# Performance work log

Hardware: AMD Instinct MI355X
Metric: run time of the kernel (lower is better)

The kernel has to match this reference:

```python
import jax, jax.numpy as jnp
import numpy as np
import math

B, L, M, D, EL, H = 128, 105, 55, 256, 3, 1
PATCH = [3, 5, 7]

def pos_embed(T, d):
    pos = jnp.arange(T, dtype=jnp.float32)[:, None]
    div = jnp.exp(jnp.arange(0, d, 2, dtype=jnp.float32) * (-math.log(10000.0) / d))
    pe = jnp.zeros((T, d), dtype=jnp.float32)
    pe = pe.at[:, 0::2].set(jnp.sin(pos * div))
    pe = pe.at[:, 1::2].set(jnp.cos(pos * div))
    return pe

def circular_conv(x, w):
    # x: [N, T, Cin], w: [Dout, Cin, 3]; Conv1d kernel 3, circular padding 1, no bias
    xc = jnp.pad(x.transpose(0, 2, 1), ((0, 0), (0, 0), (1, 1)), mode='wrap')
    y = jax.lax.conv_general_dilated(xc, w, (1,), 'VALID', dimension_numbers=('NCH', 'OIH', 'NCH'))
    return y.transpose(0, 2, 1)

def _forward(x, conv_p0, conv_n0, conv_p1, conv_n1, conv_p2, conv_n2, Wq, bq, Wk, bk):
    convs = [(conv_p0, conv_n0), (conv_p1, conv_n1), (conv_p2, conv_n2)]
    # RevIN 'norm': per-sample standardization over time; stats are detached in torch
    mean = jax.lax.stop_gradient(jnp.mean(x, axis=1, keepdims=True))
    std = jax.lax.stop_gradient(jnp.sqrt(jnp.var(x, axis=1, keepdims=True) + 1e-5))
    xr = (x - mean) / std                      # [B, L, M]
    xt = xr.transpose(0, 2, 1)                 # [B, M, L]
    dk = D // H
    scale = 1.0 / math.sqrt(dk)
    series_list, prior_list = [], []
    for i, p in enumerate(PATCH):
        n = L // p
        # patch-size branch: (b m) n p -> embed over n with in_channels=p
        x_size = circular_conv(xt.reshape(B * M, n, p), convs[i][0]) + pos_embed(n, D)
        # patch-num branch: (b m) p n -> embed over p with in_channels=n
        x_num = circular_conv(xt.reshape(B * M, p, n), convs[i][1]) + pos_embed(p, D)
        for l in range(EL):
            def attn_mean(z):
                T = z.shape[1]
                q = (z @ Wq[l] + bq[l]).reshape(B * M, T, H, dk)
                k = (z @ Wk[l] + bk[l]).reshape(B * M, T, H, dk)
                a = jax.nn.softmax(scale * jnp.einsum('blhe,bshe->bhls', q, k), axis=-1)
                # fuse: mean over channel BEFORE expanding to window size
                # (repeat/tile commutes with the channel-mean, avoids [B*M,H,L,L])
                return a.reshape(B, M, H, T, T).mean(axis=1)   # [B, H, T, T]
            a_size = attn_mean(x_size)                          # [B, H, n, n]
            # einops repeat '(m rm) (n rn)': element-wise contiguous repeat
            series_list.append(jnp.repeat(jnp.repeat(a_size, p, axis=-2), p, axis=-1))
            a_num = attn_mean(x_num)                            # [B, H, p, p]
            # torch .repeat: tiling
            prior_list.append(jnp.tile(a_num, (1, 1, n, n)))
    # order: patch-major, layer-minor (matches the flattened lists)
    return jnp.stack(series_list), jnp.stack(prior_list)        # each [9, B, H, L, L]

def setup_inputs():
    key = jax.random.key(0)
    ks = jax.random.split(key, 12)
    s = 0.05
    inp = {"x": jax.random.normal(ks[0], (B, L, M), jnp.float32)}
    for i, p in enumerate(PATCH):
        inp[f"conv_p{i}"] = s * jax.random.normal(ks[1 + 2 * i], (D, p, 3), jnp.float32)
        inp[f"conv_n{i}"] = s * jax.random.normal(ks[2 + 2 * i], (D, L // p, 3), jnp.float32)
    inp["Wq"] = s * jax.random.normal(ks[7], (EL, D, D), jnp.float32)
    inp["bq"] = jnp.zeros((EL, D), jnp.float32)
    inp["Wk"] = s * jax.random.normal(ks[8], (EL, D, D), jnp.float32)
    inp["bk"] = jnp.zeros((EL, D), jnp.float32)
    return inp

def reference(x, conv_p0, conv_n0, conv_p1, conv_n1, conv_p2, conv_n2, Wq, bq, Wk, bk):
    return _forward(x, conv_p0, conv_n0, conv_p1, conv_n1, conv_p2, conv_n2, Wq, bq, Wk, bk)
```

## Files before the change

### kernel.cpp

```cpp
#include <hip/hip_runtime.h>
#include <hip/hip_bf16.h>

#define B_ 128
#define L_ 105
#define M_ 55
#define D_ 256
#define NCOMBO 18

#define WS_XT    0
#define WS_PE    739200
#define WS_LEFT  761216
#define WS_RIGHT 1258880
#define WS_MM    1756544
#define WS_MP    761216
#define WS_ACC   1258880
#define LR_STRIDE 27648
#define MM_STRIDE 11664
#define MP_STRIDE 12544
#define ACC_TOT  758016

#define WS_LRP        1966592
#define LRP_KZ_STRIDE 27648
#define LRP_C_STRIDE  110592
#define LRP_HALF      1990656
#define WS_NEED_BYTES ((size_t)(WS_LRP + 2 * LRP_HALF) * 4)

__constant__ int c_peOff[6] = {0, 35, 38, 59, 64, 79};
__constant__ int c_accbase[18] = {0,1225,2450, 3675,3684,3693, 3702,4143,4584,
                                  5025,5050,5075, 5100,5325,5550, 5775,5824,5873};

__device__ __forceinline__ void combo_dims(int c, int& i, int& br, int& l,
                                           int& p, int& n, int& Cin, int& T, int& J) {
    i = c / 6; br = (c % 6) / 3; l = c % 3;
    p = 3 + 2 * i;
    n = L_ / p;
    Cin = br ? n : p;
    T   = br ? p : n;
    J = 3 * Cin;
}

__device__ __forceinline__ float dot4(float4 a, float4 b) {
    return a.x * b.x + a.y * b.y + a.z * b.z + a.w * b.w;
}

__global__ void revin_kernel(const float* __restrict__ x, float* __restrict__ ws) {
    int bm = blockIdx.x; int b = bm / M_; int m = bm % M_;
    int tid = threadIdx.x;
    __shared__ float s1[128], s2[128];
    float v = 0.f;
    if (tid < L_) v = x[(b * L_ + tid) * M_ + m];
    s1[tid] = v; s2[tid] = v * v;
    __syncthreads();
    for (int off = 64; off > 0; off >>= 1) {
        if (tid < off) { s1[tid] += s1[tid + off]; s2[tid] += s2[tid + off]; }
        __syncthreads();
    }
    float mean = s1[0] * (1.f / L_);
    float var  = s2[0] * (1.f / L_) - mean * mean;
    float rstd = rsqrtf(var + 1e-5f);
    if (tid < L_) ws[WS_XT + bm * L_ + tid] = (v - mean) * rstd;
}

__global__ void pe_kernel(float* __restrict__ ws) {
    int bi = blockIdx.x;
    int i = bi / 2, br = bi % 2;
    int p = 3 + 2 * i, n = L_ / p;
    int T = br ? p : n;
    int d = threadIdx.x;
    float divv = expf(-(float)(d & ~1) * (logf(10000.f) / (float)D_));
    float* base = ws + WS_PE + c_peOff[bi] * D_;
    for (int t = 0; t < T; ++t) {
        float arg = (float)t * divv;
        base[t * D_ + d] = (d & 1) ? cosf(arg) : sinf(arg);
    }
}

__global__ __launch_bounds__(256) void lr2_kernel(
                          const float* __restrict__ w0, const float* __restrict__ w1,
                          const float* __restrict__ w2c, const float* __restrict__ w3,
                          const float* __restrict__ w4, const float* __restrict__ w5,
                          const float* __restrict__ Wq, const float* __restrict__ bq,
                          const float* __restrict__ Wk, const float* __restrict__ bk,
                          float* __restrict__ ws) {
    int c = blockIdx.x;
    int i, br, l, p, n, Cin, T, J; combo_dims(c, i, br, l, p, n, Cin, T, J);
    int Mdim = J + T;
    int r0 = blockIdx.y * 8;
    if (r0 >= Mdim) return;
    int kz = blockIdx.z;
    int d0 = kz * 64;
    int wi = i * 2 + br;
    const float* conv = (wi == 0) ? w0 : (wi == 1) ? w1 : (wi == 2) ? w2c
                       : (wi == 3) ? w3 : (wi == 4) ? w4 : w5;
    __shared__ float S[8][64];
    int tid = threadIdx.x;
    for (int idx = tid; idx < 8 * 64; idx += 256) {
        int rr = idx >> 6, dd = idx & 63;
        int row = r0 + rr; float val = 0.f;
        int d = d0 + dd;
        if (row < J) val = conv[d * J + row];
        else if (row < Mdim) val = ws[WS_PE + (c_peOff[wi] + (row - J)) * D_ + d];
        S[rr][dd] = val;
    }
    __syncthreads();
    const float* wqp = Wq + l * D_ * D_;
    const float* wkp = Wk + l * D_ * D_;
    float accL[8], accR[8];
#pragma unroll
    for (int rr = 0; rr < 8; ++rr) { accL[rr] = 0.f; accR[rr] = 0.f; }
    int o = tid;
#pragma unroll 8
    for (int dd = 0; dd < 64; ++dd) {
        int d = d0 + dd;
        float wqv = wqp[d * D_ + o];
        float wkv = wkp[d * D_ + o];
#pragma unroll
        for (int rr = 0; rr < 8; ++rr) {
            float sv = S[rr][dd];
            accL[rr] += sv * wqv;
            accR[rr] += sv * wkv;
        }
    }
    float bqv = (kz == 0) ? bq[l * D_ + o] : 0.f;
    float bkv = (kz == 0) ? bk[l * D_ + o] : 0.f;
    float* Lp = ws + WS_LRP + c * LRP_C_STRIDE + kz * LRP_KZ_STRIDE;
    float* Rp = Lp + LRP_HALF;
#pragma unroll
    for (int rr = 0; rr < 8; ++rr) {
        int row = r0 + rr;
        if (row < Mdim) {
            float aq = (row >= J) ? bqv : 0.f;
            float ak = (row >= J) ? bkv : 0.f;
            Lp[row * D_ + o] = accL[rr] + aq;
            Rp[row * D_ + o] = accR[rr] + ak;
        }
    }
}

__global__ __launch_bounds__(256) void lr_kernel(
                          const float* __restrict__ w0, const float* __restrict__ w1,
                          const float* __restrict__ w2c, const float* __restrict__ w3,
                          const float* __restrict__ w4, const float* __restrict__ w5,
                          const float* __restrict__ Wq, const float* __restrict__ bq,
                          const float* __restrict__ Wk, const float* __restrict__ bk,
                          float* __restrict__ ws) {
    int c = blockIdx.x;
    int i, br, l, p, n, Cin, T, J; combo_dims(c, i, br, l, p, n, Cin, T, J);
    int Mdim = J + T;
    int r0 = blockIdx.y * 4;
    if (r0 >= Mdim) return;
    int wi = i * 2 + br;
    const float* conv = (wi == 0) ? w0 : (wi == 1) ? w1 : (wi == 2) ? w2c
                       : (wi == 3) ? w3 : (wi == 4) ? w4 : w5;
    __shared__ float S[4][256];
    int tid = threadIdx.x;
    for (int idx = tid; idx < 4 * 256; idx += 256) {
        int rr = idx >> 8, dd = idx & 255;
        int row = r0 + rr; float val = 0.f;
        if (row < J) val = conv[dd * J + row];
        else if (row < Mdim) val = ws[WS_PE + (c_peOff[wi] + (row - J)) * D_ + dd];
        S[rr][dd] = val;
    }
    __syncthreads();
    const float* wqp = Wq + l * D_ * D_;
    const float* wkp = Wk + l * D_ * D_;
    float accL[4], accR[4];
#pragma unroll
    for (int rr = 0; rr < 4; ++rr) { accL[rr] = 0.f; accR[rr] = 0.f; }
    int o = tid;
#pragma unroll 8
    for (int d = 0; d < D_; ++d) {
        float wqv = wqp[d * D_ + o];
        float wkv = wkp[d * D_ + o];
#pragma unroll
        for (int rr = 0; rr < 4; ++rr) {
            float sv = S[rr][d];
            accL[rr] += sv * wqv;
            accR[rr] += sv * wkv;
        }
    }
    float bqv = bq[l * D_ + o], bkv = bk[l * D_ + o];
#pragma unroll
    for (int rr = 0; rr < 4; ++rr) {
        int row = r0 + rr;
        if (row < Mdim) {
            float aq = (row >= J) ? bqv : 0.f;
            float ak = (row >= J) ? bkv : 0.f;
            ws[WS_LEFT  + c * LR_STRIDE + row * D_ + o] = accL[rr] + aq;
            ws[WS_RIGHT + c * LR_STRIDE + row * D_ + o] = accR[rr] + ak;
        }
    }
}

__global__ void mm_kernel(float* __restrict__ ws, int use_partial) {
    int c = blockIdx.x;
    int i, br, l, p, n, Cin, T, J; combo_dims(c, i, br, l, p, n, Cin, T, J);
    int Mdim = J + T;
    int tr = blockIdx.y / 7, tc = blockIdx.y % 7;
    int r0 = tr * 16, c0 = tc * 16;
    if (r0 >= Mdim || c0 >= Mdim) return;
    __shared__ __align__(16) float Lb[16][260], Rb[16][260];
    int tid = threadIdx.x;
    if (use_partial) {
        const float* Lp = ws + WS_LRP + c * LRP_C_STRIDE;
        const float* Rp = Lp + LRP_HALF;
        for (int idx = tid; idx < 16 * 256; idx += 256) {
            int rr = idx >> 8, d = idx & 255;
            int rL = r0 + rr, rR = c0 + rr;
            float lv = 0.f, rv = 0.f;
            if (rL < Mdim) {
                int base = rL * D_ + d;
                lv = Lp[base] + Lp[base + LRP_KZ_STRIDE]
                   + Lp[base + 2 * LRP_KZ_STRIDE] + Lp[base + 3 * LRP_KZ_STRIDE];
            }
            if (rR < Mdim) {
                int base = rR * D_ + d;
                rv = Rp[base] + Rp[base + LRP_KZ_STRIDE]
                   + Rp[base + 2 * LRP_KZ_STRIDE] + Rp[base + 3 * LRP_KZ_STRIDE];
            }
            Lb[rr][d] = lv; Rb[rr][d] = rv;
        }
    } else {
        for (int idx = tid; idx < 16 * 256; idx += 256) {
            int rr = idx >> 8, d = idx & 255;
            int rL = r0 + rr, rR = c0 + rr;
            Lb[rr][d] = (rL < Mdim) ? ws[WS_LEFT  + c * LR_STRIDE + rL * D_ + d] : 0.f;
            Rb[rr][d] = (rR < Mdim) ? ws[WS_RIGHT + c * LR_STRIDE + rR * D_ + d] : 0.f;
        }
    }
    __syncthreads();
    int rr = tid / 16, cc = tid % 16;
    const float4* lrow = (const float4*)(&Lb[rr][0]);
    const float4* rrow = (const float4*)(&Rb[cc][0]);
    float acc = 0.f;
#pragma unroll 8
    for (int d4 = 0; d4 < 64; ++d4) {
        float4 a = lrow[d4], bb = rrow[d4];
        acc += a.x * bb.x + a.y * bb.y + a.z * bb.z + a.w * bb.w;
    }
    int r = r0 + rr, cth = c0 + cc;
    if (r < Mdim && cth < Mdim)
        ws[WS_MM + c * MM_STRIDE + r * Mdim + cth] = acc;
}

__global__ void pack_kernel(float* __restrict__ ws) {
    int c = blockIdx.x;
    int i, br, l, p, n, Cin, T, J; combo_dims(c, i, br, l, p, n, Cin, T, J);
    int Mdim = J + T;
    int Cinp = (Cin + 3) & ~3;
    int Jp = 3 * Cinp;
    int T4 = (T + 3) & ~3;
    int W = Jp + T4;
    const float* MMc = ws + WS_MM + c * MM_STRIDE;
    float* Mp = ws + WS_MP + c * MP_STRIDE;
    for (int e = threadIdx.x; e < W * W; e += 256) {
        int r = e / W, o = e % W;
        int srcr = -1, srcc = -1;
        bool brow = false;
        if (r < Jp) {
            int k = r / Cinp, cin = r % Cinp;
            if (cin < Cin) srcr = cin * 3 + k;
        } else {
            int t = r - Jp;
            if (t < T) { srcr = J + t; brow = true; }
        }
        if (o < Jp) {
            int k2 = o / Cinp, cin2 = o % Cinp;
            if (cin2 < Cin) srcc = cin2 * 3 + k2;
        } else {
            int s = o - Jp;
            if (s < T) srcc = J + s;
        }
        float val;
        if (srcr >= 0 && srcc >= 0) val = MMc[srcr * Mdim + srcc];
        else if (brow && o >= Jp && srcc < 0) val = -1e30f;
        else val = 0.f;
        Mp[e] = val;
    }
}

__global__ void zero_acc(float* __restrict__ ws) {
    int idx = blockIdx.x * 256 + threadIdx.x;
    if (idx < ACC_TOT / 4) {
        float4 z; z.x = 0.f; z.y = 0.f; z.z = 0.f; z.w = 0.f;
        ((float4*)(ws + WS_ACC))[idx] = z;
    }
}

template<int P, int BR>
__global__ __launch_bounds__(256) void attn2(const float* __restrict__ ws,
                                             float* __restrict__ wsw) {
    constexpr int N    = L_ / P;
    constexpr int Cin  = BR ? N : P;
    constexpr int T    = BR ? P : N;
    constexpr int Cinp = (Cin + 3) & ~3;
    constexpr int Jp   = 3 * Cinp;
    constexpr int JP4  = Jp / 4;
    constexpr int T4   = (T + 3) & ~3;
    constexpr int W    = Jp + T4;
    constexpr int W4   = W / 4;
    constexpr int WP4  = W4 + 1;
    constexpr int WP   = WP4 * 4;
    constexpr int ST   = T4 + 1;
    constexpr int II   = (P - 3) / 2;
    constexpr int MC   = BR ? (P == 3 ? 12 : 8) : (P == 7 ? 8 : 4);
    constexpr int TH   = (BR == 0 && P == 3) ? 2 : 1;
    constexpr int TSUB = (T + TH - 1) / TH;
    constexpr int NT   = (MC / 4) * TSUB * W4;
    constexpr int TPB  = (NT + 255) / 256;
    constexpr int MCQ  = MC / 4;
    constexpr int CQ   = Cinp / 4;
    constexpr int CQP  = CQ | 1;
    constexpr int S4N  = T4 / 4;
    constexpr int XTR4 = Cinp * MCQ + 1;

    constexpr int OFF_X2A = 0;
    constexpr int SZ_X2A  = MC * T * CQP * 4;
    constexpr int OFF_G   = OFF_X2A + SZ_X2A;
    constexpr int SZ_G    = MC * TSUB * WP;
    constexpr int OFF_X2T = OFF_G + SZ_G;
    constexpr int SZ_X2T  = T * XTR4 * 4;
    constexpr int OFF_MS  = OFF_X2T + SZ_X2T;
    constexpr int SZ_MSL  = Cinp * W;
    constexpr int SZ_S    = MC * TSUB * ST;
    constexpr int SZ_MS   = (SZ_MSL > SZ_S) ? SZ_MSL : SZ_S;
    constexpr int OFF_MSL = OFF_MS;
    constexpr int OFF_S   = OFF_MS;
    constexpr int TOT     = OFF_MS + SZ_MS;
    static_assert(TOT * 4 <= 65536, "LDS budget");

    __shared__ __align__(16) float smem[TOT];
    const int tid = threadIdx.x;
    const int b = blockIdx.x;
    const int zz = blockIdx.y;
    const int sp = zz / TH;
    const int th = zz % TH;
    const int t0 = th * TSUB;
    const int TC = (T - t0 < TSUB) ? (T - t0) : TSUB;
    const int m0 = sp * MC;
    const int vm = (M_ - m0 < MC) ? (M_ - m0) : MC;

    for (int e = tid; e < MC * T * CQP * 4; e += 256) {
        int cin  = e % (CQP * 4);
        int trow = (e / (CQP * 4)) % T;
        int mcol = e / (CQP * 4 * T);
        float v = 0.f;
        if (cin < Cin && m0 + mcol < M_)
            v = ws[WS_XT + (size_t)(b * M_ + m0 + mcol) * L_ + trow * Cin + cin];
        smem[OFF_X2A + e] = v;
    }
    for (int e = tid; e < T * XTR4 * 4; e += 256) {
        int w    = e % (XTR4 * 4);
        int trow = e / (XTR4 * 4);
        float v = 0.f;
        if (w < Cinp * MC) {
            int mcol = w % MC, cin = w / MC;
            if (cin < Cin && m0 + mcol < M_)
                v = ws[WS_XT + (size_t)(b * M_ + m0 + mcol) * L_ + trow * Cin + cin];
        }
        smem[OFF_X2T + e] = v;
    }
    __syncthreads();

    const float4* X2T4 = (const float4*)(smem + OFF_X2T);
    const float4* X2A4 = (const float4*)(smem + OFF_X2A);
    float4*       MSL4 = (float4*)(smem + OFF_MSL);
    float4*       G4w  = (float4*)(smem + OFF_G);
    const float4* G4   = (const float4*)(smem + OFF_G);

    for (int l = 0; l < 3; ++l) {
        const int c = II * 6 + BR * 3 + l;
        const float*  Mpg  = ws + WS_MP + c * MP_STRIDE;
        const float4* Mpg4 = (const float4*)Mpg;

        float a[TPB][4][4];
#pragma unroll
        for (int tt = 0; tt < TPB; ++tt) {
            int q = tid + tt * 256;
            if (q < NT) {
                int o4 = q % W4, tl = (q / W4) % TSUB;
                if (tl < TC) {
                    float4 bv = Mpg4[(Jp + t0 + tl) * W4 + o4];
#pragma unroll
                    for (int am = 0; am < 4; ++am) {
                        a[tt][am][0] = bv.x; a[tt][am][1] = bv.y;
                        a[tt][am][2] = bv.z; a[tt][am][3] = bv.w;
                    }
                }
            }
        }
        for (int k = 0; k < 3; ++k) {
            for (int e = tid; e < Cinp * W4; e += 256)
                MSL4[e] = Mpg4[k * Cinp * W4 + e];
            __syncthreads();
#pragma unroll
            for (int tt = 0; tt < TPB; ++tt) {
                int q = tid + tt * 256;
                if (q < NT) {
                    int o4 = q % W4, tl = (q / W4) % TSUB, m4 = q / (W4 * TSUB);
                    if (tl < TC) {
                        int trow = t0 + tl + k - 1;
                        if (trow < 0) trow += T;
                        if (trow >= T) trow -= T;
                        const float4* xp = X2T4 + trow * XTR4 + m4;
                        const float4* mp = MSL4 + o4;
#pragma unroll 4
                        for (int cin = 0; cin < Cinp; ++cin) {
                            float4 x4 = xp[cin * MCQ];
                            float4 mv = mp[cin * W4];
#pragma unroll
                            for (int aq = 0; aq < 4; ++aq) {
                                float m = (aq == 0) ? mv.x : (aq == 1) ? mv.y
                                        : (aq == 2) ? mv.z : mv.w;
                                a[tt][0][aq] += x4.x * m;
                                a[tt][1][aq] += x4.y * m;
                                a[tt][2][aq] += x4.z * m;
                                a[tt][3][aq] += x4.w * m;
                            }
                        }
                    }
                }
            }
            __syncthreads();
        }
#pragma unroll
        for (int tt = 0; tt < TPB; ++tt) {
            int q = tid + tt * 256;
            if (q < NT) {
                int o4 = q % W4, tl = (q / W4) % TSUB, m4 = q / (W4 * TSUB);
                if (tl < TC) {
#pragma unroll
                    for (int am = 0; am < 4; ++am) {
                        float4 o;
                        o.x = a[tt][am][0]; o.y = a[tt][am][1];
                        o.z = a[tt][am][2]; o.w = a[tt][am][3];
                        G4w[((m4 * 4 + am) * TSUB + tl) * WP4 + o4] = o;
                    }
                }
            }
        }
        __syncthreads();

        for (int it = tid; it < MC * TSUB * S4N; it += 256) {
            int tl = it % TSUB;
            int s4 = (it / TSUB) % S4N;
            int mc = it / (TSUB * S4N);
            if (tl >= TC) continue;
            int grow = (mc * TSUB + tl) * WP4;
            float4 bi = G4[grow + JP4 + s4];
            float acc[4] = {bi.x, bi.y, bi.z, bi.w};
#pragma unroll 2
            for (int cinq = 0; cinq < CQ; ++cinq) {
                float4 xr[6];
#pragma unroll
                for (int kk = 0; kk < 6; ++kk) {
                    int r = s4 * 4 - 1 + kk;
                    if (r < 0) r += T;
                    if (r >= T) r -= T;
                    xr[kk] = X2A4[(mc * T + r) * CQP + cinq];
                }
#pragma unroll
                for (int k = 0; k < 3; ++k) {
                    float4 g = G4[grow + k * CQ + cinq];
#pragma unroll
                    for (int q = 0; q < 4; ++q) {
                        float4 x4 = xr[q + k];
                        acc[q] += g.x * x4.x + g.y * x4.y + g.z * x4.z + g.w * x4.w;
                    }
                }
            }
#pragma unroll
            for (int q = 0; q < 4; ++q)
                smem[OFF_S + (mc * TSUB + tl) * ST + s4 * 4 + q] = 0.0625f * acc[q];
        }
        __syncthreads();

        for (int rid = tid; rid < MC * TSUB; rid += 256) {
            int mc = rid / TSUB, tl = rid % TSUB;
            if (tl >= TC) continue;
            int base = OFF_S + (mc * TSUB + tl) * ST;
            float pr[T4];
#pragma unroll
            for (int s = 0; s < T4; ++s) pr[s] = smem[base + s];
            float mx = -1e30f;
#pragma unroll
            for (int s = 0; s < T4; ++s) mx = fmaxf(mx, pr[s]);
            float sum = 0.f;
#pragma unroll
            for (int s = 0; s < T4; ++s) { pr[s] = __expf(pr[s] - mx); sum += pr[s]; }
            float inv = 1.f / sum;
#pragma unroll
            for (int s = 0; s < T; ++s) smem[base + s] = pr[s] * inv;
        }
        __syncthreads();

        float* accp = wsw + WS_ACC + c_accbase[c] * 128 + b * T * T;
        for (int e = tid; e < TC * T; e += 256) {
            int tl = e / T, s = e % T;
            float v = 0.f;
            for (int mc = 0; mc < vm; ++mc)
                v += smem[OFF_S + (mc * TSUB + tl) * ST + s];
            atomicAdd(&accp[(t0 + tl) * T + s], v);
        }
        __syncthreads();
    }
}

template<int P, int BR>
__device__ __forceinline__ void expand_body(const float* __restrict__ acc,
                                            float* __restrict__ outp) {
    constexpr int T = BR ? P : (L_ / P);
    for (int idx = threadIdx.x; idx < L_ * L_; idx += 256) {
        int r = idx / L_, c2 = idx % L_;
        int rt = BR ? (r % P) : (r / P);
        int ct = BR ? (c2 % P) : (c2 / P);
        outp[idx] = acc[rt * T + ct];
    }
}

__global__ __launch_bounds__(256) void expand_kernel(const float* __restrict__ ws,
                                                     float* __restrict__ out) {
    int c = blockIdx.x, b = blockIdx.y;
    int i = c / 6, br = (c % 6) / 3, l = c % 3;
    int p = 3 + 2 * i;
    int T = br ? p : (L_ / p);
    __shared__ float sAcc[1232];
    int abase = c_accbase[c] * 128 + b * T * T;
    for (int idx = threadIdx.x; idx < T * T; idx += 256)
        sAcc[idx] = ws[WS_ACC + abase + idx] * (1.f / (float)M_);
    __syncthreads();
    float* outp = out + ((size_t)(br * 9 + i * 3 + l) * B_ + (size_t)b) * (size_t)(L_ * L_);
    int key = i * 2 + br;
    switch (key) {
        case 0: expand_body<3, 0>(sAcc, outp); break;
        case 1: expand_body<3, 1>(sAcc, outp); break;
        case 2: expand_body<5, 0>(sAcc, outp); break;
        case 3: expand_body<5, 1>(sAcc, outp); break;
        case 4: expand_body<7, 0>(sAcc, outp); break;
        case 5: expand_body<7, 1>(sAcc, outp); break;
    }
}

extern "C" void kernel_launch(void* const* d_in, const int* in_sizes, int n_in,
                              void* d_out, int out_size, void* d_ws, size_t ws_size,
                              hipStream_t stream) {
    const float* x   = (const float*)d_in[0];
    const float* cp0 = (const float*)d_in[1];
    const float* cn0 = (const float*)d_in[2];
    const float* cp1 = (const float*)d_in[3];
    const float* cn1 = (const float*)d_in[4];
    const float* cp2 = (const float*)d_in[5];
    const float* cn2 = (const float*)d_in[6];
    const float* Wq  = (const float*)d_in[7];
    const float* bq  = (const float*)d_in[8];
    const float* Wk  = (const float*)d_in[9];
    const float* bk  = (const float*)d_in[10];
    float* ws = (float*)d_ws;
    float* out = (float*)d_out;

    const int use_partial = (ws_size >= WS_NEED_BYTES) ? 1 : 0;

    hipLaunchKernelGGL(revin_kernel, dim3(B_ * M_), dim3(128), 0, stream, x, ws);
    hipLaunchKernelGGL(pe_kernel, dim3(6), dim3(256), 0, stream, ws);
    if (use_partial) {
        hipLaunchKernelGGL(lr2_kernel, dim3(NCOMBO, 14, 4), dim3(256), 0, stream,
                           cp0, cn0, cp1, cn1, cp2, cn2, Wq, bq, Wk, bk, ws);
    } else {
        hipLaunchKernelGGL(lr_kernel, dim3(NCOMBO, 27), dim3(256), 0, stream,
                           cp0, cn0, cp1, cn1, cp2, cn2, Wq, bq, Wk, bk, ws);
    }
    hipLaunchKernelGGL(mm_kernel, dim3(NCOMBO, 49), dim3(256), 0, stream, ws, use_partial);
    hipLaunchKernelGGL(pack_kernel, dim3(NCOMBO), dim3(256), 0, stream, ws);
    hipLaunchKernelGGL(zero_acc, dim3((ACC_TOT / 4 + 255) / 256), dim3(256), 0, stream, ws);

    hipLaunchKernelGGL((attn2<3, 0>), dim3(B_, 28), dim3(256), 0, stream, ws, ws);
    hipLaunchKernelGGL((attn2<3, 1>), dim3(B_, 5),  dim3(256), 0, stream, ws, ws);
    hipLaunchKernelGGL((attn2<5, 0>), dim3(B_, 14), dim3(256), 0, stream, ws, ws);
    hipLaunchKernelGGL((attn2<5, 1>), dim3(B_, 7),  dim3(256), 0, stream, ws, ws);
    hipLaunchKernelGGL((attn2<7, 0>), dim3(B_, 7),  dim3(256), 0, stream, ws, ws);
    hipLaunchKernelGGL((attn2<7, 1>), dim3(B_, 7),  dim3(256), 0, stream, ws, ws);

    hipLaunchKernelGGL(expand_kernel, dim3(NCOMBO, B_), dim3(256), 0, stream, ws, out);
}
```

Measured before the change: 490.2 us.

## Fuse attention launches into one grid and parallelize layers across blocks

Replaces the six per-patch attention launches with one flat-grid kernel. Block ranges are mapped to each patch/branch variant, and each encoder layer goes to its own block instead of a loop inside the block. The T split is widened to the P=5 and P=7 size branches, and the patch-num branch reads the projection matrix straight from global memory instead of staging it in LDS. Together these shrink the shared-memory footprint and raise occupancy and block-level parallelism. The cost is that each layer's block reloads and restages the input tiles.

```diff
diff --git a/kernel.cpp b/kernel.cpp
--- a/kernel.cpp
+++ b/kernel.cpp
@@ -37,10 +37,6 @@
     Cin = br ? n : p;
     T   = br ? p : n;
     J = 3 * Cin;
-}
-
-__device__ __forceinline__ float dot4(float4 a, float4 b) {
-    return a.x * b.x + a.y * b.y + a.z * b.z + a.w * b.w;
 }
 
 __global__ void revin_kernel(const float* __restrict__ x, float* __restrict__ ws) {
@@ -287,9 +283,11 @@
     }
 }
 
-template<int P, int BR>
-__global__ __launch_bounds__(256) void attn2(const float* __restrict__ ws,
-                                             float* __restrict__ wsw) {
+template<int P, int BR, int TH>
+__device__ __forceinline__ void attn_body(float* __restrict__ smem,
+                                          const float* __restrict__ ws,
+                                          float* __restrict__ wsw,
+                                          const int b, const int l, const int zz) {
     constexpr int N    = L_ / P;
     constexpr int Cin  = BR ? N : P;
     constexpr int T    = BR ? P : N;
@@ -304,10 +302,9 @@
     constexpr int ST   = T4 + 1;
     constexpr int II   = (P - 3) / 2;
     constexpr int MC   = BR ? (P == 3 ? 12 : 8) : (P == 7 ? 8 : 4);
-    constexpr int TH   = (BR == 0 && P == 3) ? 2 : 1;
     constexpr int TSUB = (T + TH - 1) / TH;
     constexpr int NT   = (MC / 4) * TSUB * W4;
-    constexpr int TPB  = (NT + 255) / 256;
+    static_assert(NT <= 256, "single-pass G tile");
     constexpr int MCQ  = MC / 4;
     constexpr int CQ   = Cinp / 4;
     constexpr int CQP  = CQ | 1;
@@ -320,25 +317,26 @@
     constexpr int SZ_G    = MC * TSUB * WP;
     constexpr int OFF_X2T = OFF_G + SZ_G;
     constexpr int SZ_X2T  = T * XTR4 * 4;
-    constexpr int OFF_MS  = OFF_X2T + SZ_X2T;
-    constexpr int SZ_MSL  = Cinp * W;
+    constexpr int OFF_MSL = OFF_X2T + SZ_X2T;
+    constexpr int SZ_MSL  = BR ? 0 : Cinp * W;
+    constexpr int OFF_S   = OFF_X2T;
     constexpr int SZ_S    = MC * TSUB * ST;
-    constexpr int SZ_MS   = (SZ_MSL > SZ_S) ? SZ_MSL : SZ_S;
-    constexpr int OFF_MSL = OFF_MS;
-    constexpr int OFF_S   = OFF_MS;
-    constexpr int TOT     = OFF_MS + SZ_MS;
-    static_assert(TOT * 4 <= 65536, "LDS budget");
-
-    __shared__ __align__(16) float smem[TOT];
+    constexpr int END_A   = OFF_MSL + SZ_MSL;
+    constexpr int END_B   = OFF_S + SZ_S;
+    constexpr int TOT     = (END_A > END_B) ? END_A : END_B;
+    static_assert(TOT <= 6968, "fused LDS budget");
+
     const int tid = threadIdx.x;
-    const int b = blockIdx.x;
-    const int zz = blockIdx.y;
     const int sp = zz / TH;
     const int th = zz % TH;
     const int t0 = th * TSUB;
     const int TC = (T - t0 < TSUB) ? (T - t0) : TSUB;
+    const int c  = II * 6 + BR * 3 + l;
     const int m0 = sp * MC;
     const int vm = (M_ - m0 < MC) ? (M_ - m0) : MC;
+
+    const float*  Mpg  = ws + WS_MP + c * MP_STRIDE;
+    const float4* Mpg4 = (const float4*)Mpg;
 
     for (int e = tid; e < MC * T * CQP * 4; e += 256) {
         int cin  = e % (CQP * 4);
@@ -368,141 +366,176 @@
     float4*       G4w  = (float4*)(smem + OFF_G);
     const float4* G4   = (const float4*)(smem + OFF_G);
 
-    for (int l = 0; l < 3; ++l) {
-        const int c = II * 6 + BR * 3 + l;
-        const float*  Mpg  = ws + WS_MP + c * MP_STRIDE;
-        const float4* Mpg4 = (const float4*)Mpg;
-
-        float a[TPB][4][4];
-#pragma unroll
-        for (int tt = 0; tt < TPB; ++tt) {
-            int q = tid + tt * 256;
-            if (q < NT) {
-                int o4 = q % W4, tl = (q / W4) % TSUB;
-                if (tl < TC) {
-                    float4 bv = Mpg4[(Jp + t0 + tl) * W4 + o4];
-#pragma unroll
-                    for (int am = 0; am < 4; ++am) {
-                        a[tt][am][0] = bv.x; a[tt][am][1] = bv.y;
-                        a[tt][am][2] = bv.z; a[tt][am][3] = bv.w;
-                    }
-                }
-            }
-        }
+    const int q  = tid;
+    const int o4 = q % W4;
+    const int tl = (q / W4) % TSUB;
+    const int m4 = q / (W4 * TSUB);
+    const bool act = (q < NT) && (tl < TC);
+    float a[4][4];
+    if (act) {
+        float4 bv = Mpg4[(Jp + t0 + tl) * W4 + o4];
+#pragma unroll
+        for (int am = 0; am < 4; ++am) {
+            a[am][0] = bv.x; a[am][1] = bv.y;
+            a[am][2] = bv.z; a[am][3] = bv.w;
+        }
+    }
+    if constexpr (BR == 0) {
         for (int k = 0; k < 3; ++k) {
             for (int e = tid; e < Cinp * W4; e += 256)
                 MSL4[e] = Mpg4[k * Cinp * W4 + e];
             __syncthreads();
-#pragma unroll
-            for (int tt = 0; tt < TPB; ++tt) {
-                int q = tid + tt * 256;
-                if (q < NT) {
-                    int o4 = q % W4, tl = (q / W4) % TSUB, m4 = q / (W4 * TSUB);
-                    if (tl < TC) {
-                        int trow = t0 + tl + k - 1;
-                        if (trow < 0) trow += T;
-                        if (trow >= T) trow -= T;
-                        const float4* xp = X2T4 + trow * XTR4 + m4;
-                        const float4* mp = MSL4 + o4;
+            if (act) {
+                int trow = t0 + tl + k - 1;
+                if (trow < 0) trow += T;
+                if (trow >= T) trow -= T;
+                const float4* xp = X2T4 + trow * XTR4 + m4;
+                const float4* mp = MSL4 + o4;
 #pragma unroll 4
-                        for (int cin = 0; cin < Cinp; ++cin) {
-                            float4 x4 = xp[cin * MCQ];
-                            float4 mv = mp[cin * W4];
-#pragma unroll
-                            for (int aq = 0; aq < 4; ++aq) {
-                                float m = (aq == 0) ? mv.x : (aq == 1) ? mv.y
-                                        : (aq == 2) ? mv.z : mv.w;
-                                a[tt][0][aq] += x4.x * m;
-                                a[tt][1][aq] += x4.y * m;
-                                a[tt][2][aq] += x4.z * m;
-                                a[tt][3][aq] += x4.w * m;
-                            }
-                        }
+                for (int cin = 0; cin < Cinp; ++cin) {
+                    float4 x4 = xp[cin * MCQ];
+                    float4 mv = mp[cin * W4];
+#pragma unroll
+                    for (int aq = 0; aq < 4; ++aq) {
+                        float m = (aq == 0) ? mv.x : (aq == 1) ? mv.y
+                                : (aq == 2) ? mv.z : mv.w;
+                        a[0][aq] += x4.x * m;
+                        a[1][aq] += x4.y * m;
+                        a[2][aq] += x4.z * m;
+                        a[3][aq] += x4.w * m;
                     }
                 }
             }
             __syncthreads();
         }
-#pragma unroll
-        for (int tt = 0; tt < TPB; ++tt) {
-            int q = tid + tt * 256;
-            if (q < NT) {
-                int o4 = q % W4, tl = (q / W4) % TSUB, m4 = q / (W4 * TSUB);
-                if (tl < TC) {
-#pragma unroll
-                    for (int am = 0; am < 4; ++am) {
-                        float4 o;
-                        o.x = a[tt][am][0]; o.y = a[tt][am][1];
-                        o.z = a[tt][am][2]; o.w = a[tt][am][3];
-                        G4w[((m4 * 4 + am) * TSUB + tl) * WP4 + o4] = o;
+    } else {
+        if (act) {
+#pragma unroll
+            for (int k = 0; k < 3; ++k) {
+                int trow = t0 + tl + k - 1;
+                if (trow < 0) trow += T;
+                if (trow >= T) trow -= T;
+                const float4* xp = X2T4 + trow * XTR4 + m4;
+                const float4* mp = Mpg4 + k * Cinp * W4 + o4;
+#pragma unroll 4
+                for (int cin = 0; cin < Cinp; ++cin) {
+                    float4 x4 = xp[cin * MCQ];
+                    float4 mv = mp[cin * W4];
+#pragma unroll
+                    for (int aq = 0; aq < 4; ++aq) {
+                        float m = (aq == 0) ? mv.x : (aq == 1) ? mv.y
+                                : (aq == 2) ? mv.z : mv.w;
+                        a[0][aq] += x4.x * m;
+                        a[1][aq] += x4.y * m;
+                        a[2][aq] += x4.z * m;
+                        a[3][aq] += x4.w * m;
                     }
                 }
             }
         }
-        __syncthreads();
-
-        for (int it = tid; it < MC * TSUB * S4N; it += 256) {
-            int tl = it % TSUB;
-            int s4 = (it / TSUB) % S4N;
-            int mc = it / (TSUB * S4N);
-            if (tl >= TC) continue;
-            int grow = (mc * TSUB + tl) * WP4;
-            float4 bi = G4[grow + JP4 + s4];
-            float acc[4] = {bi.x, bi.y, bi.z, bi.w};
+    }
+    if (act) {
+#pragma unroll
+        for (int am = 0; am < 4; ++am) {
+            float4 o;
+            o.x = a[am][0]; o.y = a[am][1];
+            o.z = a[am][2]; o.w = a[am][3];
+            G4w[((m4 * 4 + am) * TSUB + tl) * WP4 + o4] = o;
+        }
+    }
+    __syncthreads();
+
+    for (int it = tid; it < MC * TSUB * S4N; it += 256) {
+        int stl = it % TSUB;
+        int s4  = (it / TSUB) % S4N;
+        int mc  = it / (TSUB * S4N);
+        if (stl >= TC) continue;
+        int grow = (mc * TSUB + stl) * WP4;
+        float4 bi = G4[grow + JP4 + s4];
+        float acc[4] = {bi.x, bi.y, bi.z, bi.w};
 #pragma unroll 2
-            for (int cinq = 0; cinq < CQ; ++cinq) {
-                float4 xr[6];
-#pragma unroll
-                for (int kk = 0; kk < 6; ++kk) {
-                    int r = s4 * 4 - 1 + kk;
-                    if (r < 0) r += T;
-                    if (r >= T) r -= T;
-                    xr[kk] = X2A4[(mc * T + r) * CQP + cinq];
-                }
-#pragma unroll
-                for (int k = 0; k < 3; ++k) {
-                    float4 g = G4[grow + k * CQ + cinq];
-#pragma unroll
-                    for (int q = 0; q < 4; ++q) {
-                        float4 x4 = xr[q + k];
-                        acc[q] += g.x * x4.x + g.y * x4.y + g.z * x4.z + g.w * x4.w;
-                    }
+        for (int cinq = 0; cinq < CQ; ++cinq) {
+            float4 xr[6];
+#pragma unroll
+            for (int kk = 0; kk < 6; ++kk) {
+                int r = s4 * 4 - 1 + kk;
+                if (r < 0) r += T;
+                if (r >= T) r -= T;
+                xr[kk] = X2A4[(mc * T + r) * CQP + cinq];
+            }
+#pragma unroll
+            for (int k = 0; k < 3; ++k) {
+                float4 g = G4[grow + k * CQ + cinq];
+#pragma unroll
+                for (int qq = 0; qq < 4; ++qq) {
+                    float4 x4 = xr[qq + k];
+                    acc[qq] += g.x * x4.x + g.y * x4.y + g.z * x4.z + g.w * x4.w;
                 }
             }
-#pragma unroll
-            for (int q = 0; q < 4; ++q)
-                smem[OFF_S + (mc * TSUB + tl) * ST + s4 * 4 + q] = 0.0625f * acc[q];
-        }
-        __syncthreads();
-
-        for (int rid = tid; rid < MC * TSUB; rid += 256) {
-            int mc = rid / TSUB, tl = rid % TSUB;
-            if (tl >= TC) continue;
-            int base = OFF_S + (mc * TSUB + tl) * ST;
-            float pr[T4];
-#pragma unroll
-            for (int s = 0; s < T4; ++s) pr[s] = smem[base + s];
-            float mx = -1e30f;
-#pragma unroll
-            for (int s = 0; s < T4; ++s) mx = fmaxf(mx, pr[s]);
-            float sum = 0.f;
-#pragma unroll
-            for (int s = 0; s < T4; ++s) { pr[s] = __expf(pr[s] - mx); sum += pr[s]; }
-            float inv = 1.f / sum;
-#pragma unroll
-            for (int s = 0; s < T; ++s) smem[base + s] = pr[s] * inv;
-        }
-        __syncthreads();
-
-        float* accp = wsw + WS_ACC + c_accbase[c] * 128 + b * T * T;
-        for (int e = tid; e < TC * T; e += 256) {
-            int tl = e / T, s = e % T;
-            float v = 0.f;
-            for (int mc = 0; mc < vm; ++mc)
-                v += smem[OFF_S + (mc * TSUB + tl) * ST + s];
-            atomicAdd(&accp[(t0 + tl) * T + s], v);
-        }
-        __syncthreads();
+        }
+#pragma unroll
+        for (int qq = 0; qq < 4; ++qq)
+            smem[OFF_S + (mc * TSUB + stl) * ST + s4 * 4 + qq] = 0.0625f * acc[qq];
+    }
+    __syncthreads();
+
+    for (int rid = tid; rid < MC * TSUB; rid += 256) {
+        int mc = rid / TSUB, stl = rid % TSUB;
+        if (stl >= TC) continue;
+        int base = OFF_S + (mc * TSUB + stl) * ST;
+        float pr[T4];
+#pragma unroll
+        for (int s = 0; s < T4; ++s) pr[s] = smem[base + s];
+        float mx = -1e30f;
+#pragma unroll
+        for (int s = 0; s < T4; ++s) mx = fmaxf(mx, pr[s]);
+        float sum = 0.f;
+#pragma unroll
+        for (int s = 0; s < T4; ++s) { pr[s] = __expf(pr[s] - mx); sum += pr[s]; }
+        float inv = 1.f / sum;
+#pragma unroll
+        for (int s = 0; s < T; ++s) smem[base + s] = pr[s] * inv;
+    }
+    __syncthreads();
+
+    float* accp = wsw + WS_ACC + c_accbase[c] * 128 + b * T * T;
+    for (int e = tid; e < TC * T; e += 256) {
+        int stl = e / T, s = e % T;
+        float v = 0.f;
+        for (int mc = 0; mc < vm; ++mc)
+            v += smem[OFF_S + (mc * TSUB + stl) * ST + s];
+        atomicAdd(&accp[(t0 + stl) * T + s], v);
+    }
+}
+
+#define ATTN_TOTAL_BLOCKS 34176
+__global__ __launch_bounds__(256) void attn_fused(const float* __restrict__ ws,
+                                                  float* __restrict__ wsw) {
+    __shared__ __align__(16) float smem[6968];
+    int bid = blockIdx.x;
+    if (bid < 1920) {
+        int zz = bid % 5, l = (bid / 5) % 3, b = bid / 15;
+        attn_body<3, 1, 1>(smem, ws, wsw, b, l, zz);
+    } else if (bid < 4608) {
+        bid -= 1920;
+        int zz = bid % 7, l = (bid / 7) % 3, b = bid / 21;
+        attn_body<5, 1, 1>(smem, ws, wsw, b, l, zz);
+    } else if (bid < 7296) {
+        bid -= 4608;
+        int zz = bid % 7, l = (bid / 7) % 3, b = bid / 21;
+        attn_body<7, 1, 1>(smem, ws, wsw, b, l, zz);
+    } else if (bid < 12672) {
+        bid -= 7296;
+        int zz = bid % 14, l = (bid / 14) % 3, b = bid / 42;
+        attn_body<7, 0, 2>(smem, ws, wsw, b, l, zz);
+    } else if (bid < 23424) {
+        bid -= 12672;
+        int zz = bid % 28, l = (bid / 28) % 3, b = bid / 84;
+        attn_body<5, 0, 2>(smem, ws, wsw, b, l, zz);
+    } else {
+        bid -= 23424;
+        int zz = bid % 28, l = (bid / 28) % 3, b = bid / 84;
+        attn_body<3, 0, 2>(smem, ws, wsw, b, l, zz);
     }
 }
 
@@ -573,12 +606,7 @@
     hipLaunchKernelGGL(pack_kernel, dim3(NCOMBO), dim3(256), 0, stream, ws);
     hipLaunchKernelGGL(zero_acc, dim3((ACC_TOT / 4 + 255) / 256), dim3(256), 0, stream, ws);
 
-    hipLaunchKernelGGL((attn2<3, 0>), dim3(B_, 28), dim3(256), 0, stream, ws, ws);
-    hipLaunchKernelGGL((attn2<3, 1>), dim3(B_, 5),  dim3(256), 0, stream, ws, ws);
-    hipLaunchKernelGGL((attn2<5, 0>), dim3(B_, 14), dim3(256), 0, stream, ws, ws);
-    hipLaunchKernelGGL((attn2<5, 1>), dim3(B_, 7),  dim3(256), 0, stream, ws, ws);
-    hipLaunchKernelGGL((attn2<7, 0>), dim3(B_, 7),  dim3(256), 0, stream, ws, ws);
-    hipLaunchKernelGGL((attn2<7, 1>), dim3(B_, 7),  dim3(256), 0, stream, ws, ws);
+    hipLaunchKernelGGL(attn_fused, dim3(ATTN_TOTAL_BLOCKS), dim3(256), 0, stream, ws, ws);
 
     hipLaunchKernelGGL(expand_kernel, dim3(NCOMBO, B_), dim3(256), 0, stream, ws, out);
 }
```

Result: slower. 501.6 us (+2.3%).
